# Optimization experiments

Measured on AMD Instinct MI355X. Metric: run time of the kernel, lower is better.

## Reference

```python
import jax, jax.numpy as jnp
import numpy as np

B, N_TOTAL, C_IN, C_OUT = 16, 50000, 5, 2
N0, N1, N2 = 20000, 5000, 1000   # nodes per dataflow block (dst sizes)
E0, E1, E2 = 320000, 80000, 16000


def setup_inputs() -> dict:
    key = jax.random.key(0)
    ks = jax.random.split(key, 12)
    x = jax.random.normal(ks[0], (B, N_TOTAL, C_IN), jnp.float32)
    n_id = jax.random.randint(ks[1], (N0,), 0, N_TOTAL)
    # intra-block edges for conv1/conv2 (constructed self-loop-free, as PyG removes them)
    src0 = jax.random.randint(ks[2], (E0,), 0, N0)
    dst0 = (src0 + jax.random.randint(ks[3], (E0,), 1, N0)) % N0
    edge_index0 = jnp.stack([src0, dst0])
    edge_index1 = jnp.stack([jax.random.randint(ks[4], (E1,), 0, N0),
                             jax.random.randint(ks[5], (E1,), 0, N1)])
    edge_index2 = jnp.stack([jax.random.randint(ks[6], (E2,), 0, N1),
                             jax.random.randint(ks[7], (E2,), 0, N2)])

    def lin(k, fi, fo):
        kw, kb = jax.random.split(k)
        bound = 1.0 / np.sqrt(fi)
        W = jax.random.uniform(kw, (fi, fo), jnp.float32, -bound, bound)
        b = jax.random.uniform(kb, (fo,), jnp.float32, -bound, bound)
        return W, b

    W1, b1 = lin(ks[8], 2 * C_IN, 6)    # concat=True -> 2*in
    W2, b2 = lin(ks[9], 2 * 6, 36)
    W3, b3 = lin(ks[10], 36, 216)
    W4, b4 = lin(ks[11], 216, C_OUT)
    return dict(x=x, n_id=n_id, edge_index0=edge_index0, edge_index1=edge_index1,
                edge_index2=edge_index2, W1=W1, b1=b1, W2=W2, b2=b2,
                W3=W3, b3=b3, W4=W4, b4=b4)


def _sage(x_src, edge_index, num_dst, W, b, concat, normalize, x_self=None):
    """Old-style PyG SAGEConv with aggr='mean', node_dim=1."""
    src, dst = edge_index[0], edge_index[1]
    msgs = x_src[:, src, :]                                        # [B, E, C]
    agg = jnp.zeros((x_src.shape[0], num_dst, x_src.shape[2]), x_src.dtype)
    agg = agg.at[:, dst, :].add(msgs)                              # scatter-sum over node dim
    cnt = jnp.zeros((num_dst,), x_src.dtype).at[dst].add(1.0)
    agg = agg / jnp.maximum(cnt, 1.0)[None, :, None]               # scatter-mean
    if concat:
        agg = jnp.concatenate([x_self, agg], axis=-1)
    out = agg @ W + b
    if normalize:
        out = out / jnp.maximum(jnp.linalg.norm(out, axis=-1, keepdims=True), 1e-12)
    return out


def reference(x, n_id, edge_index0, edge_index1, edge_index2,
              W1, b1, W2, b2, W3, b3, W4, b4):
    ar = jnp.arange(N0, dtype=edge_index0.dtype)
    ei0 = jnp.concatenate([edge_index0, jnp.stack([ar, ar])], axis=1)  # add self-loops
    xt = x[:, n_id, :]                                                  # [B, N0, C_IN]
    xt = jax.nn.relu(_sage(xt, ei0, N0, W1, b1, True, True, xt))        # [B, N0, 6]
    xt = jax.nn.relu(_sage(xt, ei0, N0, W2, b2, True, True, xt))        # [B, N0, 36]
    xt = jax.nn.relu(_sage(xt, edge_index1, N1, W3, b3, False, False))  # [B, N1, 216]
    xt = _sage(xt, edge_index2, N2, W4, b4, False, False)               # [B, N2, C_OUT]
    return xt
```

## Files before the change

kernel.cpp:

```cpp
#include <hip/hip_runtime.h>
#include <hip/hip_fp16.h>

#define NTOT 50000
#define N0 20000
#define N1 5000
#define N2 1000
#define E0C 320000
#define E1C 80000
#define E2C 16000
#define BKT 64

#define ZERO_BLOCKS ((N0 + N1 + N2 + 255) / 256)
#define PREP_BLOCKS 56
#define EDGE_BLOCKS ((E0C + E1C + E2C + 255) / 256)
#define GATH_BLOCKS ((N0 * 16 + 255) / 256)

typedef _Float16 half8 __attribute__((ext_vector_type(8)));
typedef float floatx4 __attribute__((ext_vector_type(4)));

__global__ void init_kernel(int* __restrict__ cur, const float* __restrict__ W3,
                            _Float16* __restrict__ W3B) {
    int blk = blockIdx.x;
    if (blk < ZERO_BLOCKS) {
        int i = blk * 256 + threadIdx.x;
        if (i < N0 + N1 + N2) cur[i] = 0;
    } else {
        int idx = (blk - ZERO_BLOCKS) * 256 + threadIdx.x;
        if (idx < 14 * 2 * 64 * 8) {
            int j = idx & 7;
            int l = (idx >> 3) & 63;
            int ks = (idx >> 9) & 1;
            int t = idx >> 10;
            int k = ks * 32 + (l >> 4) * 8 + j;
            int col = t * 16 + (l & 15);
            float v = (k < 36 && col < 216) ? W3[k * 216 + col] : 0.f;
            W3B[idx] = (_Float16)v;
        }
    }
}

__global__ void scatter_gather(const int* __restrict__ ei0, const int* __restrict__ ei1,
                               const int* __restrict__ ei2,
                               int* __restrict__ cur0, int* __restrict__ cur1, int* __restrict__ cur2,
                               int* __restrict__ ss0, int* __restrict__ ss1, int* __restrict__ ss2,
                               const float* __restrict__ x, const int* __restrict__ n_id,
                               __half* __restrict__ xt0h) {
    int blk = blockIdx.x;
    if (blk < EDGE_BLOCKS) {
        int i = blk * 256 + threadIdx.x;
        if (i < E0C) {
            int d = ei0[E0C + i];
            int pos = atomicAdd(&cur0[d], 1);
            ss0[d * BKT + pos] = ei0[i];
        } else if (i < E0C + E1C) {
            int j = i - E0C;
            int d = ei1[E1C + j];
            int pos = atomicAdd(&cur1[d], 1);
            ss1[d * BKT + pos] = ei1[j];
        } else if (i < E0C + E1C + E2C) {
            int j = i - E0C - E1C;
            int d = ei2[E2C + j];
            int pos = atomicAdd(&cur2[d], 1);
            ss2[d * BKT + pos] = ei2[j];
        }
    } else {
        int idx = (blk - EDGE_BLOCKS) * 256 + threadIdx.x;
        if (idx < N0 * 16) {
            int n = idx >> 4, b = idx & 15;
            const float* p = x + (size_t)b * (NTOT * 5) + (size_t)n_id[n] * 5;
            union { __half h[8]; uint4 u; } pk;
#pragma unroll
            for (int c = 0; c < 5; c++) pk.h[c] = __float2half_rn(p[c]);
            pk.h[5] = __half(0.f);
            pk.h[6] = __half(0.f);
            pk.h[7] = __half(0.f);
            *(uint4*)(xt0h + (size_t)n * 128 + b * 8) = pk.u;
        }
    }
}

__global__ __launch_bounds__(256) void sage1_kernel(
    const __half* __restrict__ xt0h, const int* __restrict__ deg, const int* __restrict__ ssrc,
    const float* __restrict__ W, const float* __restrict__ bias, __half* __restrict__ xt1h) {
    int gtid = blockIdx.x * blockDim.x + threadIdx.x;
    int wid = gtid >> 6;
    int lane = threadIdx.x & 63;
    int d = wid * 4 + (lane >> 4);
    int b = lane & 15;
    if (d >= N0) return;
    union { uint4 u; __half2 h2[4]; } sp;
    sp.u = *(const uint4*)(xt0h + (size_t)d * 128 + b * 8);
    float2 s01 = __half22float2(sp.h2[0]);
    float2 s23 = __half22float2(sp.h2[1]);
    float2 s4x = __half22float2(sp.h2[2]);
    float xs[5] = {s01.x, s01.y, s23.x, s23.y, s4x.x};
    float a[5] = {xs[0], xs[1], xs[2], xs[3], xs[4]};
    int e0 = d * BKT, e1 = e0 + deg[d];
    int e = e0;
    union { uint4 u; __half2 h2[4]; } pk[8];
    for (; e + 7 < e1; e += 8) {
#pragma unroll
        for (int u = 0; u < 8; u++)
            pk[u].u = *(const uint4*)(xt0h + (size_t)ssrc[e + u] * 128 + b * 8);
#pragma unroll
        for (int u = 0; u < 8; u++) {
            float2 v01 = __half22float2(pk[u].h2[0]);
            float2 v23 = __half22float2(pk[u].h2[1]);
            float2 v4x = __half22float2(pk[u].h2[2]);
            a[0] += v01.x; a[1] += v01.y; a[2] += v23.x; a[3] += v23.y; a[4] += v4x.x;
        }
    }
    for (; e + 3 < e1; e += 4) {
#pragma unroll
        for (int u = 0; u < 4; u++)
            pk[u].u = *(const uint4*)(xt0h + (size_t)ssrc[e + u] * 128 + b * 8);
#pragma unroll
        for (int u = 0; u < 4; u++) {
            float2 v01 = __half22float2(pk[u].h2[0]);
            float2 v23 = __half22float2(pk[u].h2[1]);
            float2 v4x = __half22float2(pk[u].h2[2]);
            a[0] += v01.x; a[1] += v01.y; a[2] += v23.x; a[3] += v23.y; a[4] += v4x.x;
        }
    }
    for (; e < e1; e++) {
        pk[0].u = *(const uint4*)(xt0h + (size_t)ssrc[e] * 128 + b * 8);
        float2 v01 = __half22float2(pk[0].h2[0]);
        float2 v23 = __half22float2(pk[0].h2[1]);
        float2 v4x = __half22float2(pk[0].h2[2]);
        a[0] += v01.x; a[1] += v01.y; a[2] += v23.x; a[3] += v23.y; a[4] += v4x.x;
    }
    float inv = 1.f / (float)(e1 - e0 + 1);
#pragma unroll
    for (int c = 0; c < 5; c++) a[c] *= inv;
    float o[6];
#pragma unroll
    for (int j = 0; j < 6; j++) {
        float acc = bias[j];
#pragma unroll
        for (int i = 0; i < 5; i++) acc += xs[i] * W[i * 6 + j];
#pragma unroll
        for (int i = 0; i < 5; i++) acc += a[i] * W[(5 + i) * 6 + j];
        o[j] = acc;
    }
    float nrm = 0.f;
#pragma unroll
    for (int j = 0; j < 6; j++) nrm += o[j] * o[j];
    float r = 1.f / fmaxf(sqrtf(nrm), 1e-12f);
    union { __half h[8]; uint4 u; } pko;
#pragma unroll
    for (int j = 0; j < 6; j++) pko.h[j] = __float2half_rn(fmaxf(o[j] * r, 0.f));
    pko.h[6] = __half(0.f);
    pko.h[7] = __half(0.f);
    *(uint4*)(xt1h + (size_t)d * 128 + b * 8) = pko.u;
}

__global__ __launch_bounds__(256) void sage2_kernel(
    const __half* __restrict__ xt1h, const int* __restrict__ deg, const int* __restrict__ ssrc,
    const float* __restrict__ W, const float* __restrict__ bias, __half* __restrict__ xt2h) {
    int gtid = blockIdx.x * blockDim.x + threadIdx.x;
    int wid = gtid >> 6;
    int lane = threadIdx.x & 63;
    int d = wid * 4 + (lane >> 4);
    int b = lane & 15;
    if (d >= N0) return;
    const __half2* ps = (const __half2*)(xt1h + (size_t)d * 128 + b * 8);
    float2 s01 = __half22float2(ps[0]);
    float2 s23 = __half22float2(ps[1]);
    float2 s45 = __half22float2(ps[2]);
    float xs[6] = {s01.x, s01.y, s23.x, s23.y, s45.x, s45.y};
    float a[6] = {xs[0], xs[1], xs[2], xs[3], xs[4], xs[5]};
    int e0 = d * BKT, e1 = e0 + deg[d];
    int e = e0;
    union { uint4 u; __half2 h2[4]; } pk[8];
    for (; e + 7 < e1; e += 8) {
#pragma unroll
        for (int u = 0; u < 8; u++)
            pk[u].u = *(const uint4*)(xt1h + (size_t)ssrc[e + u] * 128 + b * 8);
#pragma unroll
        for (int u = 0; u < 8; u++) {
#pragma unroll
            for (int j = 0; j < 3; j++) {
                float2 v = __half22float2(pk[u].h2[j]);
                a[2 * j] += v.x;
                a[2 * j + 1] += v.y;
            }
        }
    }
    for (; e + 3 < e1; e += 4) {
#pragma unroll
        for (int u = 0; u < 4; u++)
            pk[u].u = *(const uint4*)(xt1h + (size_t)ssrc[e + u] * 128 + b * 8);
#pragma unroll
        for (int u = 0; u < 4; u++) {
#pragma unroll
            for (int j = 0; j < 3; j++) {
                float2 v = __half22float2(pk[u].h2[j]);
                a[2 * j] += v.x;
                a[2 * j + 1] += v.y;
            }
        }
    }
    for (; e < e1; e++) {
        pk[0].u = *(const uint4*)(xt1h + (size_t)ssrc[e] * 128 + b * 8);
#pragma unroll
        for (int j = 0; j < 3; j++) {
            float2 v = __half22float2(pk[0].h2[j]);
            a[2 * j] += v.x;
            a[2 * j + 1] += v.y;
        }
    }
    float inv = 1.f / (float)(e1 - e0 + 1);
#pragma unroll
    for (int c = 0; c < 6; c++) a[c] *= inv;
    float o[36];
#pragma unroll
    for (int j = 0; j < 36; j++) {
        float acc = bias[j];
#pragma unroll
        for (int i = 0; i < 6; i++) acc += xs[i] * W[i * 36 + j];
#pragma unroll
        for (int i = 0; i < 6; i++) acc += a[i] * W[(6 + i) * 36 + j];
        o[j] = acc;
    }
    float nrm = 0.f;
#pragma unroll
    for (int j = 0; j < 36; j++) nrm += o[j] * o[j];
    float r = 1.f / fmaxf(sqrtf(nrm), 1e-12f);
    __half* pd = xt2h + (size_t)d * 576 + b;
#pragma unroll
    for (int j = 0; j < 36; j++) pd[j * 16] = __float2half_rn(fmaxf(o[j] * r, 0.f));
}

__global__ __launch_bounds__(256) void sage3_kernel(
    const __half* __restrict__ xt2h, const int* __restrict__ deg, const int* __restrict__ ssrc,
    const _Float16* __restrict__ W3B, const float* __restrict__ b3,
    const float* __restrict__ W4, float* __restrict__ y) {
    __shared__ float sPart[4][576];
    __shared__ float sT[1024];
    __shared__ float sRed[4][32];
    int t = threadIdx.x;
    int w = t >> 6, q = t & 63;
    int d = blockIdx.x;
    int e0 = d * BKT, e1 = e0 + deg[d];

    float acc[16];
#pragma unroll
    for (int i = 0; i < 16; i++) acc[i] = 0.f;
    const uint4* base = (const uint4*)xt2h;
    union { uint4 u; __half2 h2[4]; } c0, c1, d0, d1;
    int e = e0 + w;
    for (; e + 4 < e1; e += 8) {
        int s0 = ssrc[e], s1 = ssrc[e + 4];
        const uint4* p0 = base + (size_t)s0 * 72;
        const uint4* p1 = base + (size_t)s1 * 72;
        c0.u = p0[q];
        c1.u = p1[q];
        if (q < 8) { d0.u = p0[64 + q]; d1.u = p1[64 + q]; }
#pragma unroll
        for (int j = 0; j < 4; j++) {
            float2 f0 = __half22float2(c0.h2[j]);
            float2 f1 = __half22float2(c1.h2[j]);
            acc[2 * j] += f0.x + f1.x;
            acc[2 * j + 1] += f0.y + f1.y;
        }
        if (q < 8) {
#pragma unroll
            for (int j = 0; j < 4; j++) {
                float2 f0 = __half22float2(d0.h2[j]);
                float2 f1 = __half22float2(d1.h2[j]);
                acc[8 + 2 * j] += f0.x + f1.x;
                acc[9 + 2 * j] += f0.y + f1.y;
            }
        }
    }
    for (; e < e1; e += 4) {
        const uint4* p0 = base + (size_t)ssrc[e] * 72;
        c0.u = p0[q];
        if (q < 8) d0.u = p0[64 + q];
#pragma unroll
        for (int j = 0; j < 4; j++) {
            float2 f = __half22float2(c0.h2[j]);
            acc[2 * j] += f.x;
            acc[2 * j + 1] += f.y;
        }
        if (q < 8) {
#pragma unroll
            for (int j = 0; j < 4; j++) {
                float2 f = __half22float2(d0.h2[j]);
                acc[8 + 2 * j] += f.x;
                acc[9 + 2 * j] += f.y;
            }
        }
    }
#pragma unroll
    for (int j = 0; j < 8; j++) sPart[w][q * 8 + j] = acc[j];
    if (q < 8) {
#pragma unroll
        for (int j = 0; j < 8; j++) sPart[w][512 + q * 8 + j] = acc[8 + j];
    }
    __syncthreads();
    float inv = 1.f / fmaxf((float)(e1 - e0), 1.f);
    for (int i = t; i < 1024; i += 256)
        sT[i] = (i < 576) ? (sPart[0][i] + sPart[1][i] + sPart[2][i] + sPart[3][i]) * inv : 0.f;
    __syncthreads();

    int lb = q & 15;
    int hg = q >> 4;
    half8 aF[2];
#pragma unroll
    for (int ks = 0; ks < 2; ks++) {
#pragma unroll
        for (int j = 0; j < 8; j++) {
            int k = ks * 32 + hg * 8 + j;
            aF[ks][j] = (_Float16)sT[k * 16 + lb];
        }
    }
    float y0[4] = {0.f, 0.f, 0.f, 0.f};
    float y1[4] = {0.f, 0.f, 0.f, 0.f};
#pragma unroll
    for (int tt = 0; tt < 4; tt++) {
        int tile = w + 4 * tt;
        if (tile >= 14) break;
        floatx4 cacc = {0.f, 0.f, 0.f, 0.f};
#pragma unroll
        for (int ks = 0; ks < 2; ks++) {
            half8 bF = *(const half8*)(W3B + ((size_t)(tile * 2 + ks) * 64 + q) * 8);
            cacc = __builtin_amdgcn_mfma_f32_16x16x32_f16(aF[ks], bF, cacc, 0, 0, 0);
        }
        int col = tile * 16 + lb;
        float bj  = (col < 216) ? b3[col] : 0.f;
        float w40 = (col < 216) ? W4[col * 2] : 0.f;
        float w41 = (col < 216) ? W4[col * 2 + 1] : 0.f;
#pragma unroll
        for (int r = 0; r < 4; r++) {
            float vv = fmaxf(cacc[r] + bj, 0.f);
            y0[r] = fmaf(vv, w40, y0[r]);
            y1[r] = fmaf(vv, w41, y1[r]);
        }
    }
#pragma unroll
    for (int m = 1; m <= 8; m <<= 1) {
#pragma unroll
        for (int r = 0; r < 4; r++) {
            y0[r] += __shfl_xor(y0[r], m, 64);
            y1[r] += __shfl_xor(y1[r], m, 64);
        }
    }
    if (lb == 0) {
#pragma unroll
        for (int r = 0; r < 4; r++) {
            int row = hg * 4 + r;
            sRed[w][row * 2 + 0] = y0[r];
            sRed[w][row * 2 + 1] = y1[r];
        }
    }
    __syncthreads();
    if (t < 32) y[(size_t)d * 32 + t] = sRed[0][t] + sRed[1][t] + sRed[2][t] + sRed[3][t];
}

__global__ void final_kernel(const float* __restrict__ y, const int* __restrict__ deg,
                             const int* __restrict__ ssrc, const float* __restrict__ b4,
                             float* __restrict__ out) {
    int idx = blockIdx.x * blockDim.x + threadIdx.x;
    if (idx >= N2 * 16) return;
    int d = idx >> 4, b = idx & 15;
    int e0 = d * BKT, e1 = e0 + deg[d];
    float s0 = 0.f, s1 = 0.f;
    for (int e = e0; e < e1; e++) {
        int s = ssrc[e];
        const float2 v = *(const float2*)(y + (size_t)s * 32 + b * 2);
        s0 += v.x; s1 += v.y;
    }
    float inv = 1.f / fmaxf((float)(e1 - e0), 1.f);
    out[b * (N2 * 2) + d * 2 + 0] = s0 * inv + b4[0];
    out[b * (N2 * 2) + d * 2 + 1] = s1 * inv + b4[1];
}

extern "C" void kernel_launch(void* const* d_in, const int* in_sizes, int n_in,
                              void* d_out, int out_size, void* d_ws, size_t ws_size,
                              hipStream_t stream) {
    const float* x   = (const float*)d_in[0];
    const int* n_id  = (const int*)d_in[1];
    const int* ei0   = (const int*)d_in[2];
    const int* ei1   = (const int*)d_in[3];
    const int* ei2   = (const int*)d_in[4];
    const float* W1  = (const float*)d_in[5];
    const float* b1  = (const float*)d_in[6];
    const float* W2  = (const float*)d_in[7];
    const float* b2  = (const float*)d_in[8];
    const float* W3  = (const float*)d_in[9];
    const float* b3  = (const float*)d_in[10];
    const float* W4  = (const float*)d_in[11];
    const float* b4  = (const float*)d_in[12];
    float* out = (float*)d_out;

    char* ws = (char*)d_ws;
    size_t off = 0;
    auto alloc = [&](size_t bytes) -> void* {
        void* p = ws + off;
        off += (bytes + 255) & ~(size_t)255;
        return p;
    };
    __half* xt0h = (__half*)alloc((size_t)N0 * 128 * 2);
    __half* xt1h = (__half*)alloc((size_t)N0 * 128 * 2);
    __half* xt2h = (__half*)alloc((size_t)N0 * 576 * 2);
    float* yb    = (float*)alloc((size_t)N1 * 32 * 4);
    _Float16* W3B = (_Float16*)alloc((size_t)14 * 2 * 64 * 8 * 2);
    int* cur  = (int*)alloc((size_t)(N0 + N1 + N2) * 4);
    int* cur0 = cur;
    int* cur1 = cur + N0;
    int* cur2 = cur + N0 + N1;
    int* ss0 = (int*)alloc((size_t)N0 * BKT * 4);
    int* ss1 = (int*)alloc((size_t)N1 * BKT * 4);
    int* ss2 = (int*)alloc((size_t)N2 * BKT * 4);

    init_kernel<<<ZERO_BLOCKS + PREP_BLOCKS, 256, 0, stream>>>(cur, W3, W3B);
    scatter_gather<<<EDGE_BLOCKS + GATH_BLOCKS, 256, 0, stream>>>(
        ei0, ei1, ei2, cur0, cur1, cur2, ss0, ss1, ss2, x, n_id, xt0h);
    sage1_kernel<<<N0 / 16, 256, 0, stream>>>(xt0h, cur0, ss0, W1, b1, xt1h);
    sage2_kernel<<<N0 / 16, 256, 0, stream>>>(xt1h, cur0, ss0, W2, b2, xt2h);
    sage3_kernel<<<N1, 256, 0, stream>>>(xt2h, cur1, ss1, W3B, b3, W4, yb);
    final_kernel<<<(N2 * 16 + 255) / 256, 256, 0, stream>>>(yb, cur2, ss2, b4, out);
}
```

Baseline: 113.6 us.

## Split sage1 edge loop across 4 lanes per node, unroll sage3 gather by 4

sage1 now gives each destination node a full wavefront: four 16-lane groups each take every fourth edge, and their partial sums are combined with xor shuffles before the dense part runs. Only group 0 writes the result, and the grid grows to N0/4 blocks. In sage3, each wave now loads four neighbour rows per iteration instead of two, putting more gathers in flight. The aim is to shorten each node's serial edge loop and hide gather latency, at the cost of redundant dense math in sage1 and higher register pressure in sage3.

```diff
diff --git a/kernel.cpp b/kernel.cpp
--- a/kernel.cpp
+++ b/kernel.cpp
@@ -82,38 +82,25 @@
 __global__ __launch_bounds__(256) void sage1_kernel(
     const __half* __restrict__ xt0h, const int* __restrict__ deg, const int* __restrict__ ssrc,
     const float* __restrict__ W, const float* __restrict__ bias, __half* __restrict__ xt1h) {
-    int gtid = blockIdx.x * blockDim.x + threadIdx.x;
-    int wid = gtid >> 6;
-    int lane = threadIdx.x & 63;
-    int d = wid * 4 + (lane >> 4);
-    int b = lane & 15;
-    if (d >= N0) return;
+    int d = (blockIdx.x * 256 + threadIdx.x) >> 6;
+    int q = threadIdx.x & 63;
+    int es = q >> 4, b = q & 15;
     union { uint4 u; __half2 h2[4]; } sp;
     sp.u = *(const uint4*)(xt0h + (size_t)d * 128 + b * 8);
     float2 s01 = __half22float2(sp.h2[0]);
     float2 s23 = __half22float2(sp.h2[1]);
     float2 s4x = __half22float2(sp.h2[2]);
     float xs[5] = {s01.x, s01.y, s23.x, s23.y, s4x.x};
-    float a[5] = {xs[0], xs[1], xs[2], xs[3], xs[4]};
-    int e0 = d * BKT, e1 = e0 + deg[d];
-    int e = e0;
-    union { uint4 u; __half2 h2[4]; } pk[8];
-    for (; e + 7 < e1; e += 8) {
-#pragma unroll
-        for (int u = 0; u < 8; u++)
-            pk[u].u = *(const uint4*)(xt0h + (size_t)ssrc[e + u] * 128 + b * 8);
-#pragma unroll
-        for (int u = 0; u < 8; u++) {
-            float2 v01 = __half22float2(pk[u].h2[0]);
-            float2 v23 = __half22float2(pk[u].h2[1]);
-            float2 v4x = __half22float2(pk[u].h2[2]);
-            a[0] += v01.x; a[1] += v01.y; a[2] += v23.x; a[3] += v23.y; a[4] += v4x.x;
-        }
-    }
-    for (; e + 3 < e1; e += 4) {
+    float a[5] = {0.f, 0.f, 0.f, 0.f, 0.f};
+    int dg = deg[d];
+    const int e0 = d * BKT;
+    union { uint4 u; __half2 h2[4]; } pk[4];
+    int nb = dg >> 4;
+    for (int i = 0; i < nb; i++) {
+        int base = e0 + i * 16 + es;
 #pragma unroll
         for (int u = 0; u < 4; u++)
-            pk[u].u = *(const uint4*)(xt0h + (size_t)ssrc[e + u] * 128 + b * 8);
+            pk[u].u = *(const uint4*)(xt0h + (size_t)ssrc[base + 4 * u] * 128 + b * 8);
 #pragma unroll
         for (int u = 0; u < 4; u++) {
             float2 v01 = __half22float2(pk[u].h2[0]);
@@ -122,16 +109,21 @@
             a[0] += v01.x; a[1] += v01.y; a[2] += v23.x; a[3] += v23.y; a[4] += v4x.x;
         }
     }
-    for (; e < e1; e++) {
-        pk[0].u = *(const uint4*)(xt0h + (size_t)ssrc[e] * 128 + b * 8);
+    for (int e = nb * 16 + es; e < dg; e += 4) {
+        pk[0].u = *(const uint4*)(xt0h + (size_t)ssrc[e0 + e] * 128 + b * 8);
         float2 v01 = __half22float2(pk[0].h2[0]);
         float2 v23 = __half22float2(pk[0].h2[1]);
         float2 v4x = __half22float2(pk[0].h2[2]);
         a[0] += v01.x; a[1] += v01.y; a[2] += v23.x; a[3] += v23.y; a[4] += v4x.x;
     }
-    float inv = 1.f / (float)(e1 - e0 + 1);
-#pragma unroll
-    for (int c = 0; c < 5; c++) a[c] *= inv;
+#pragma unroll
+    for (int c = 0; c < 5; c++) {
+        a[c] += __shfl_xor(a[c], 16, 64);
+        a[c] += __shfl_xor(a[c], 32, 64);
+    }
+    float inv = 1.f / (float)(dg + 1);
+#pragma unroll
+    for (int c = 0; c < 5; c++) a[c] = (a[c] + xs[c]) * inv;
     float o[6];
 #pragma unroll
     for (int j = 0; j < 6; j++) {
@@ -146,12 +138,14 @@
 #pragma unroll
     for (int j = 0; j < 6; j++) nrm += o[j] * o[j];
     float r = 1.f / fmaxf(sqrtf(nrm), 1e-12f);
-    union { __half h[8]; uint4 u; } pko;
-#pragma unroll
-    for (int j = 0; j < 6; j++) pko.h[j] = __float2half_rn(fmaxf(o[j] * r, 0.f));
-    pko.h[6] = __half(0.f);
-    pko.h[7] = __half(0.f);
-    *(uint4*)(xt1h + (size_t)d * 128 + b * 8) = pko.u;
+    if (es == 0) {
+        union { __half h[8]; uint4 u; } pko;
+#pragma unroll
+        for (int j = 0; j < 6; j++) pko.h[j] = __float2half_rn(fmaxf(o[j] * r, 0.f));
+        pko.h[6] = __half(0.f);
+        pko.h[7] = __half(0.f);
+        *(uint4*)(xt1h + (size_t)d * 128 + b * 8) = pko.u;
+    }
 }
 
 __global__ __launch_bounds__(256) void sage2_kernel(
@@ -241,52 +235,61 @@
     int t = threadIdx.x;
     int w = t >> 6, q = t & 63;
     int d = blockIdx.x;
-    int e0 = d * BKT, e1 = e0 + deg[d];
+    int dg = deg[d];
+    const int e0 = d * BKT;
 
     float acc[16];
 #pragma unroll
     for (int i = 0; i < 16; i++) acc[i] = 0.f;
     const uint4* base = (const uint4*)xt2h;
-    union { uint4 u; __half2 h2[4]; } c0, c1, d0, d1;
-    int e = e0 + w;
-    for (; e + 4 < e1; e += 8) {
-        int s0 = ssrc[e], s1 = ssrc[e + 4];
-        const uint4* p0 = base + (size_t)s0 * 72;
-        const uint4* p1 = base + (size_t)s1 * 72;
-        c0.u = p0[q];
-        c1.u = p1[q];
-        if (q < 8) { d0.u = p0[64 + q]; d1.u = p1[64 + q]; }
+    union { uint4 u; __half2 h2[4]; } c[4], dx[4];
+    int nb = dg >> 4;
+    for (int i = 0; i < nb; i++) {
+        int eb = e0 + i * 16 + w;
+        const uint4* p0 = base + (size_t)ssrc[eb] * 72;
+        const uint4* p1 = base + (size_t)ssrc[eb + 4] * 72;
+        const uint4* p2 = base + (size_t)ssrc[eb + 8] * 72;
+        const uint4* p3 = base + (size_t)ssrc[eb + 12] * 72;
+        c[0].u = p0[q]; c[1].u = p1[q]; c[2].u = p2[q]; c[3].u = p3[q];
+        if (q < 8) {
+            dx[0].u = p0[64 + q]; dx[1].u = p1[64 + q];
+            dx[2].u = p2[64 + q]; dx[3].u = p3[64 + q];
+        }
+#pragma unroll
+        for (int u = 0; u < 4; u++) {
+#pragma unroll
+            for (int j = 0; j < 4; j++) {
+                float2 f = __half22float2(c[u].h2[j]);
+                acc[2 * j] += f.x;
+                acc[2 * j + 1] += f.y;
+            }
+        }
+        if (q < 8) {
+#pragma unroll
+            for (int u = 0; u < 4; u++) {
+#pragma unroll
+                for (int j = 0; j < 4; j++) {
+                    float2 f = __half22float2(dx[u].h2[j]);
+                    acc[8 + 2 * j] += f.x;
+                    acc[9 + 2 * j] += f.y;
+                }
+            }
+        }
+    }
+    for (int e = nb * 16 + w; e < dg; e += 4) {
+        const uint4* p0 = base + (size_t)ssrc[e0 + e] * 72;
+        c[0].u = p0[q];
+        if (q < 8) dx[0].u = p0[64 + q];
 #pragma unroll
         for (int j = 0; j < 4; j++) {
-            float2 f0 = __half22float2(c0.h2[j]);
-            float2 f1 = __half22float2(c1.h2[j]);
-            acc[2 * j] += f0.x + f1.x;
-            acc[2 * j + 1] += f0.y + f1.y;
-        }
-        if (q < 8) {
-#pragma unroll
-            for (int j = 0; j < 4; j++) {
-                float2 f0 = __half22float2(d0.h2[j]);
-                float2 f1 = __half22float2(d1.h2[j]);
-                acc[8 + 2 * j] += f0.x + f1.x;
-                acc[9 + 2 * j] += f0.y + f1.y;
-            }
-        }
-    }
-    for (; e < e1; e += 4) {
-        const uint4* p0 = base + (size_t)ssrc[e] * 72;
-        c0.u = p0[q];
-        if (q < 8) d0.u = p0[64 + q];
-#pragma unroll
-        for (int j = 0; j < 4; j++) {
-            float2 f = __half22float2(c0.h2[j]);
+            float2 f = __half22float2(c[0].h2[j]);
             acc[2 * j] += f.x;
             acc[2 * j + 1] += f.y;
         }
         if (q < 8) {
 #pragma unroll
             for (int j = 0; j < 4; j++) {
-                float2 f = __half22float2(d0.h2[j]);
+                float2 f = __half22float2(dx[0].h2[j]);
                 acc[8 + 2 * j] += f.x;
                 acc[9 + 2 * j] += f.y;
             }
@@ -299,7 +302,7 @@
         for (int j = 0; j < 8; j++) sPart[w][512 + q * 8 + j] = acc[8 + j];
     }
     __syncthreads();
-    float inv = 1.f / fmaxf((float)(e1 - e0), 1.f);
+    float inv = 1.f / fmaxf((float)dg, 1.f);
     for (int i = t; i < 1024; i += 256)
         sT[i] = (i < 576) ? (sPart[0][i] + sPart[1][i] + sPart[2][i] + sPart[3][i]) * inv : 0.f;
     __syncthreads();
@@ -417,7 +420,7 @@
     init_kernel<<<ZERO_BLOCKS + PREP_BLOCKS, 256, 0, stream>>>(cur, W3, W3B);
     scatter_gather<<<EDGE_BLOCKS + GATH_BLOCKS, 256, 0, stream>>>(
         ei0, ei1, ei2, cur0, cur1, cur2, ss0, ss1, ss2, x, n_id, xt0h);
-    sage1_kernel<<<N0 / 16, 256, 0, stream>>>(xt0h, cur0, ss0, W1, b1, xt1h);
+    sage1_kernel<<<N0 / 4, 256, 0, stream>>>(xt0h, cur0, ss0, W1, b1, xt1h);
     sage2_kernel<<<N0 / 16, 256, 0, stream>>>(xt1h, cur0, ss0, W2, b2, xt2h);
     sage3_kernel<<<N1, 256, 0, stream>>>(xt2h, cur1, ss1, W3B, b3, W4, yb);
     final_kernel<<<(N2 * 16 + 255) / 256, 256, 0, stream>>>(yb, cur2, ss2, b4, out);
```

Result: slower. 119.7 us (+5.4%).
